# Performance work log

Hardware: AMD Instinct MI355X
Metric: run time of the kernel (lower is better)

The kernel has to match this reference:

```python
import jax, jax.numpy as jnp
import numpy as np

B, S, H, N = 2, 2048, 1024, 16
D = H // N


def setup_inputs() -> dict:
    key = jax.random.key(0)
    k1, k2, k3 = jax.random.split(key, 3)
    # Xavier-uniform-ish init for projection weights
    lim_in = (6.0 / (H + 3 * H)) ** 0.5
    lim_out = (6.0 / (H + H)) ** 0.5
    return {
        "hidden_states": jax.random.normal(k1, (B, S, H), dtype=jnp.float32),
        "w_in": jax.random.uniform(k2, (3 * H, H), minval=-lim_in, maxval=lim_in, dtype=jnp.float32),
        "b_in": jnp.zeros((3 * H,), dtype=jnp.float32),
        "w_out": jax.random.uniform(k3, (H, H), minval=-lim_out, maxval=lim_out, dtype=jnp.float32),
        "b_out": jnp.zeros((H,), dtype=jnp.float32),
    }


def reference(hidden_states, w_in, b_in, w_out, b_out):
    b, s, h = hidden_states.shape
    qkv = hidden_states @ w_in.T + b_in  # [B,S,3H]
    q, k, v = jnp.split(qkv, 3, axis=-1)
    # [B,S,H] -> [B,N,S,D]
    def to_heads(x):
        return x.reshape(b, s, N, D).transpose(0, 2, 1, 3)
    q, k, v = to_heads(q), to_heads(k), to_heads(v)
    scale = D ** -0.5
    scores = jnp.einsum("bnqd,bnkd->bnqk", q, k) * scale  # [B,N,S,S]
    causal = jnp.triu(jnp.ones((s, s), dtype=bool), k=1)
    scores = jnp.where(causal, -jnp.inf, scores)
    attn = jax.nn.softmax(scores, axis=-1)
    out = jnp.einsum("bnqk,bnkd->bnqd", attn, v)  # [B,N,S,D]
    out = out.transpose(0, 2, 1, 3).reshape(b, s, h)
    return out @ w_out.T + b_out
```

## Files before the change

### kernel.cpp

```cpp
#include <hip/hip_runtime.h>
#include <hip/hip_bf16.h>

#define BB 2
#define SS 2048
#define HH 1024
#define NH 16
#define DD 64
#define H3 3072
#define MM (BB*SS)

typedef unsigned short u16;
typedef unsigned int u32;
typedef __attribute__((ext_vector_type(8))) short bf16x8;
typedef __attribute__((ext_vector_type(4))) float f32x4;

__device__ __forceinline__ u16 f2bf(float f) {
    union { float f; u32 u; } v; v.f = f;
    u32 u = v.u;
    u += 0x7fffu + ((u >> 16) & 1u);
    return (u16)(u >> 16);
}
__device__ __forceinline__ float bf2f(u16 h) {
    union { u32 u; float f; } v; v.u = ((u32)h) << 16;
    return v.f;
}
__device__ __forceinline__ u32 pack2bf(float a, float b) {
    __hip_bfloat162 h = __float22bfloat162_rn(float2{a, b});
    u32 u; __builtin_memcpy(&u, &h, 4);
    return u;
}
__device__ __forceinline__ void gl_lds16(const void* g, void* l) {
    __builtin_amdgcn_global_load_lds(
        (const __attribute__((address_space(1))) u32*)g,
        (__attribute__((address_space(3))) u32*)l, 16, 0, 0);
}

__global__ void cvt3bf(const float4* __restrict__ s0, uint2* __restrict__ d0, int n0,
                       const float4* __restrict__ s1, uint2* __restrict__ d1, int n1,
                       const float4* __restrict__ s2, uint2* __restrict__ d2, int n2) {
    int i = blockIdx.x * blockDim.x + threadIdx.x;
    const int tot = n0 + n1 + n2;
    for (; i < tot; i += gridDim.x * blockDim.x) {
        const float4* s; uint2* d; int j;
        if (i < n0)            { s = s0; d = d0; j = i; }
        else if (i < n0 + n1)  { s = s1; d = d1; j = i - n0; }
        else                   { s = s2; d = d2; j = i - n0 - n1; }
        float4 v = s[j];
        uint2 o; o.x = pack2bf(v.x, v.y); o.y = pack2bf(v.z, v.w);
        d[j] = o;
    }
}

template<int BN, int MODE>
__global__ __launch_bounds__(256, 2)
void gemm_k2(const u16* __restrict__ A, const u16* __restrict__ Bbf,
             const u16* __restrict__ biasbf, void* __restrict__ Cptr,
             u16* __restrict__ Qo, u16* __restrict__ Ko, u16* __restrict__ Vto,
             int M, int Nn, int K)
{
    constexpr int NFR = BN / 32;
    __shared__ __align__(16) u16 Alds[128 * 32];
    __shared__ __align__(16) u16 Blds[BN * 32];
    const int tid = threadIdx.x;
    const int w = tid >> 6, lane = tid & 63, quad = lane >> 4, l16 = lane & 15;
    const int m0 = blockIdx.x * 128, n0 = blockIdx.y * BN;
    const int wm = w >> 1, wn = w & 1;
    const int rA4 = lane >> 2, c8b = (lane & 3) * 8;

    f32x4 acc[4][NFR] = {};

    for (int k0 = 0; k0 < K; k0 += 32) {
        __syncthreads();
#pragma unroll
        for (int q = 0; q < 2; ++q) {
            int row0 = w * 32 + q * 16;
            gl_lds16(&A[(size_t)(m0 + row0 + rA4) * K + k0 + c8b], &Alds[row0 * 32]);
        }
#pragma unroll
        for (int q = 0; q < BN / 64; ++q) {
            int row0 = w * (BN / 4) + q * 16;
            gl_lds16(&Bbf[(size_t)(n0 + row0 + rA4) * K + k0 + c8b], &Blds[row0 * 32]);
        }
        __syncthreads();

        bf16x8 af[4], bfr[NFR];
#pragma unroll
        for (int mi = 0; mi < 4; ++mi)
            af[mi] = *(const bf16x8*)&Alds[(wm * 64 + mi * 16 + l16) * 32 + quad * 8];
#pragma unroll
        for (int ni = 0; ni < NFR; ++ni)
            bfr[ni] = *(const bf16x8*)&Blds[(wn * (BN / 2) + ni * 16 + l16) * 32 + quad * 8];
#pragma unroll
        for (int mi = 0; mi < 4; ++mi)
#pragma unroll
            for (int ni = 0; ni < NFR; ++ni)
                acc[mi][ni] = __builtin_amdgcn_mfma_f32_16x16x32_bf16(
                    af[mi], bfr[ni], acc[mi][ni], 0, 0, 0);
    }

#pragma unroll
    for (int mi = 0; mi < 4; ++mi) {
        int row_b = m0 + wm * 64 + mi * 16 + quad * 4;
#pragma unroll
        for (int ni = 0; ni < NFR; ++ni) {
            int col = n0 + wn * (BN / 2) + ni * 16 + l16;
            float bv = bf2f(biasbf[col]);
            if constexpr (MODE == 1) {
#pragma unroll
                for (int i = 0; i < 4; ++i)
                    ((float*)Cptr)[(size_t)(row_b + i) * Nn + col] = acc[mi][ni][i] + bv;
            } else {
                if (col < 1024) {
#pragma unroll
                    for (int i = 0; i < 4; ++i)
                        Qo[(size_t)(row_b + i) * 1024 + col] =
                            f2bf((acc[mi][ni][i] + bv) * 0.125f);
                } else if (col < 2048) {
#pragma unroll
                    for (int i = 0; i < 4; ++i)
                        Ko[(size_t)(row_b + i) * 1024 + (col - 1024)] =
                            f2bf(acc[mi][ni][i] + bv);
                } else {
                    int d = col - 2048, hh = d >> 6, dd = d & 63;
                    int b = row_b >> 11, s = row_b & 2047;
                    u16 t0 = f2bf(acc[mi][ni][0] + bv), t1 = f2bf(acc[mi][ni][1] + bv);
                    u16 t2 = f2bf(acc[mi][ni][2] + bv), t3 = f2bf(acc[mi][ni][3] + bv);
                    uint2 pk; pk.x = (u32)t0 | ((u32)t1 << 16);
                    pk.y = (u32)t2 | ((u32)t3 << 16);
                    *(uint2*)&Vto[((size_t)((b * 16 + hh) * 64 + dd)) * 2048 + s] = pk;
                }
            }
        }
    }
}

__global__ __launch_bounds__(256, 2)
void attn_v4(const u16* __restrict__ Q, const u16* __restrict__ Kb,
             const u16* __restrict__ Vt, u16* __restrict__ attn_out) {
    const int pr = blockIdx.x, h = blockIdx.y, b = blockIdx.z;
    const int tid = threadIdx.x;
    const int w = tid >> 6, lane = tid & 63, quad = lane >> 4, l16 = lane & 15;
    __shared__ __align__(16) u16 Klds[2][64 * 72];
    __shared__ __align__(16) u16 Vlds[2][64 * 72];
    const int r0 = tid >> 3, cc8 = (tid & 7) * 8;
    const int Rp = ((r0 & 4) << 2) | ((r0 & 24) >> 1) | (r0 & 3);

    for (int half = 0; half < 2; ++half) {
        const int qt = half ? pr : (31 - pr);
        const int q0 = qt * 64;
        const int T = qt + 1;

        const u16* Qb = Q  + (size_t)(b * SS + q0) * 1024 + h * 64;
        const u16* Kg = Kb + (size_t)(b * SS) * 1024 + h * 64;
        const u16* Vg = Vt + (size_t)((b * 16 + h) * 64) * 2048;

        bf16x8 qf0 = *(const bf16x8*)&Qb[(size_t)(w * 16 + l16) * 1024 + quad * 8];
        bf16x8 qf1 = *(const bf16x8*)&Qb[(size_t)(w * 16 + l16) * 1024 + 32 + quad * 8];

        f32x4 oacc[4] = {};
        float lp = 0.f;

        uint4 kr0 = *(const uint4*)&Kg[(size_t)r0 * 1024 + cc8];
        uint4 kr1 = *(const uint4*)&Kg[(size_t)(r0 + 32) * 1024 + cc8];
        uint4 vr0 = *(const uint4*)&Vg[(size_t)r0 * 2048 + cc8];
        uint4 vr1 = *(const uint4*)&Vg[(size_t)(r0 + 32) * 2048 + cc8];
        __syncthreads();
        *(uint4*)&Klds[0][Rp * 72 + cc8]        = kr0;
        *(uint4*)&Klds[0][(Rp + 32) * 72 + cc8] = kr1;
        *(uint4*)&Vlds[0][r0 * 72 + cc8]        = vr0;
        *(uint4*)&Vlds[0][(r0 + 32) * 72 + cc8] = vr1;

        for (int t = 0; t < T; ++t) {
            const int cur = t & 1;
            __syncthreads();
            if (t + 1 < T) {
                const int nv = (t + 1) * 64;
                kr0 = *(const uint4*)&Kg[(size_t)(nv + r0) * 1024 + cc8];
                kr1 = *(const uint4*)&Kg[(size_t)(nv + r0 + 32) * 1024 + cc8];
                vr0 = *(const uint4*)&Vg[(size_t)r0 * 2048 + nv + cc8];
                vr1 = *(const uint4*)&Vg[(size_t)(r0 + 32) * 2048 + nv + cc8];
            }
            f32x4 sacc[4] = {};
#pragma unroll
            for (int ni = 0; ni < 4; ++ni) {
                bf16x8 kf0 = *(const bf16x8*)&Klds[cur][(ni * 16 + l16) * 72 + quad * 8];
                bf16x8 kf1 = *(const bf16x8*)&Klds[cur][(ni * 16 + l16) * 72 + 32 + quad * 8];
                sacc[ni] = __builtin_amdgcn_mfma_f32_16x16x32_bf16(kf0, qf0, sacc[ni], 0, 0, 0);
                sacc[ni] = __builtin_amdgcn_mfma_f32_16x16x32_bf16(kf1, qf1, sacc[ni], 0, 0, 0);
            }
            u32 pk[4][2];
            if (t + 1 < T) {
#pragma unroll
                for (int ni = 0; ni < 4; ++ni) {
                    float p0 = __expf(sacc[ni][0]), p1 = __expf(sacc[ni][1]);
                    float p2 = __expf(sacc[ni][2]), p3 = __expf(sacc[ni][3]);
                    lp += (p0 + p1) + (p2 + p3);
                    pk[ni][0] = pack2bf(p0, p1);
                    pk[ni][1] = pack2bf(p2, p3);
                }
            } else {
                const int thr = w * 16 + l16;
#pragma unroll
                for (int ni = 0; ni < 4; ++ni) {
                    const int pb = 32 * (ni >> 1) + 8 * quad + 4 * (ni & 1);
                    float pv[4];
#pragma unroll
                    for (int i = 0; i < 4; ++i) {
                        float e = __expf(sacc[ni][i]);
                        pv[i] = (pb + i <= thr) ? e : 0.f;
                    }
                    lp += (pv[0] + pv[1]) + (pv[2] + pv[3]);
                    pk[ni][0] = pack2bf(pv[0], pv[1]);
                    pk[ni][1] = pack2bf(pv[2], pv[3]);
                }
            }
            union { u32 u[4]; bf16x8 v; } pf0, pf1;
            pf0.u[0] = pk[0][0]; pf0.u[1] = pk[0][1];
            pf0.u[2] = pk[1][0]; pf0.u[3] = pk[1][1];
            pf1.u[0] = pk[2][0]; pf1.u[1] = pk[2][1];
            pf1.u[2] = pk[3][0]; pf1.u[3] = pk[3][1];
#pragma unroll
            for (int ni = 0; ni < 4; ++ni) {
                bf16x8 vf0 = *(const bf16x8*)&Vlds[cur][(ni * 16 + l16) * 72 + quad * 8];
                bf16x8 vf1 = *(const bf16x8*)&Vlds[cur][(ni * 16 + l16) * 72 + 32 + quad * 8];
                oacc[ni] = __builtin_amdgcn_mfma_f32_16x16x32_bf16(pf0.v, vf0, oacc[ni], 0, 0, 0);
                oacc[ni] = __builtin_amdgcn_mfma_f32_16x16x32_bf16(pf1.v, vf1, oacc[ni], 0, 0, 0);
            }
            if (t + 1 < T) {
                const int nxt = cur ^ 1;
                *(uint4*)&Klds[nxt][Rp * 72 + cc8]        = kr0;
                *(uint4*)&Klds[nxt][(Rp + 32) * 72 + cc8] = kr1;
                *(uint4*)&Vlds[nxt][r0 * 72 + cc8]        = vr0;
                *(uint4*)&Vlds[nxt][(r0 + 32) * 72 + cc8] = vr1;
            }
        }

        lp += __shfl_xor(lp, 16, 64);
        lp += __shfl_xor(lp, 32, 64);
        float linv[4];
#pragma unroll
        for (int i = 0; i < 4; ++i)
            linv[i] = 1.0f / __shfl(lp, quad * 4 + i, 64);

        u16* ob = attn_out + (size_t)(b * SS + q0 + w * 16) * 1024 + h * 64;
#pragma unroll
        for (int ni = 0; ni < 4; ++ni)
#pragma unroll
            for (int i = 0; i < 4; ++i)
                ob[(size_t)(quad * 4 + i) * 1024 + ni * 16 + l16] =
                    f2bf(oacc[ni][i] * linv[i]);
    }
}

extern "C" void kernel_launch(void* const* d_in, const int* in_sizes, int n_in,
                              void* d_out, int out_size, void* d_ws, size_t ws_size,
                              hipStream_t stream) {
    const float* hidden = (const float*)d_in[0];
    const float* w_in   = (const float*)d_in[1];
    const float* b_in   = (const float*)d_in[2];
    const float* w_out  = (const float*)d_in[3];
    const float* b_out  = (const float*)d_in[4];
    float* out = (float*)d_out;

    char* ws = (char*)d_ws;
    u16* hid_bf  = (u16*)d_out;
    u16* wi_bf   = (u16*)ws;
    u16* bi_bf   = (u16*)(ws + 6291456);
    u16* attn_ws = (u16*)ws;
    u16* Qbuf    = (u16*)(ws + 8388608);
    u16* wo_bf   = (u16*)(ws + 8388608);
    u16* bo_bf   = (u16*)(ws + 8388608 + 2097152);
    u16* Kbuf    = (u16*)(ws + 16777216);
    u16* Vtbuf   = (u16*)(ws + 25165824);

    cvt3bf<<<dim3(2048), dim3(256), 0, stream>>>(
        (const float4*)hidden, (uint2*)hid_bf, 1048576,
        (const float4*)w_in,   (uint2*)wi_bf,  786432,
        (const float4*)b_in,   (uint2*)bi_bf,  768);
    gemm_k2<128, 2><<<dim3(32, 24), dim3(256), 0, stream>>>(
        hid_bf, wi_bf, bi_bf, nullptr, Qbuf, Kbuf, Vtbuf, MM, H3, HH);
    attn_v4<<<dim3(16, NH, BB), dim3(256), 0, stream>>>(
        Qbuf, Kbuf, Vtbuf, attn_ws);
    cvt3bf<<<dim3(512), dim3(256), 0, stream>>>(
        (const float4*)w_out, (uint2*)wo_bf, 262144,
        (const float4*)b_out, (uint2*)bo_bf, 256,
        nullptr, nullptr, 0);
    gemm_k2<64, 1><<<dim3(32, 16), dim3(256), 0, stream>>>(
        attn_ws, wo_bf, bo_bf, out, nullptr, nullptr, nullptr, MM, HH, HH);
}
```

Measured before the change: 178.9 us.

## Stage attention K/V tiles with direct global-to-LDS loads and XOR swizzle

The attention kernel now moves K and V tiles straight from global memory into LDS with global_load_lds instead of staging them through registers. Padded 72-element LDS rows become unpadded 64-element rows with an XOR swizzle to avoid bank conflicts. The grid is flattened to 1D with a remapping that interleaves heads and batches across block IDs. This aims to cut register pressure and VGPR-to-LDS store instructions, at the cost of relying on the global_load_lds prefetch being complete at the next barrier and on intricate swizzle index math.

```diff
diff --git a/kernel.cpp b/kernel.cpp
--- a/kernel.cpp
+++ b/kernel.cpp
@@ -33,6 +33,9 @@
     __builtin_amdgcn_global_load_lds(
         (const __attribute__((address_space(1))) u32*)g,
         (__attribute__((address_space(3))) u32*)l, 16, 0, 0);
+}
+__device__ __forceinline__ int ginv(int R) {
+    return (R & 35) | ((R & 8) << 1) | ((R & 4) << 1) | ((R & 16) >> 2);
 }
 
 __global__ void cvt3bf(const float4* __restrict__ s0, uint2* __restrict__ d0, int n0,
@@ -135,15 +138,24 @@
 }
 
 __global__ __launch_bounds__(256, 2)
-void attn_v4(const u16* __restrict__ Q, const u16* __restrict__ Kb,
+void attn_v5(const u16* __restrict__ Q, const u16* __restrict__ Kb,
              const u16* __restrict__ Vt, u16* __restrict__ attn_out) {
-    const int pr = blockIdx.x, h = blockIdx.y, b = blockIdx.z;
+    const int bid = blockIdx.x;
+    const int r8 = bid & 7, qq = bid >> 3;
+    const int pr = qq >> 2, g = (qq & 3) * 8 + r8;
+    const int h = g & 15, b = g >> 4;
     const int tid = threadIdx.x;
     const int w = tid >> 6, lane = tid & 63, quad = lane >> 4, l16 = lane & 15;
-    __shared__ __align__(16) u16 Klds[2][64 * 72];
-    __shared__ __align__(16) u16 Vlds[2][64 * 72];
-    const int r0 = tid >> 3, cc8 = (tid & 7) * 8;
-    const int Rp = ((r0 & 4) << 2) | ((r0 & 24) >> 1) | (r0 & 3);
+    __shared__ __align__(16) u16 Klds[2][64 * 64];
+    __shared__ __align__(16) u16 Vlds[2][64 * 64];
+
+    const int sl = lane >> 3, cch = lane & 7;
+    const int rho0 = (2 * w) * 8 + sl, rho1 = (2 * w + 1) * 8 + sl;
+    const int gcs = (cch ^ sl) * 8;
+    const int kg0 = ginv(rho0), kg1 = ginv(rho1);
+    const int ls0 = (2 * w) * 512, ls1 = (2 * w + 1) * 512;
+    const int xk0 = (quad ^ (l16 & 7)) * 8;
+    const int xk1 = ((quad + 4) ^ (l16 & 7)) * 8;
 
     for (int half = 0; half < 2; ++half) {
         const int qt = half ? pr : (31 - pr);
@@ -154,37 +166,34 @@
         const u16* Kg = Kb + (size_t)(b * SS) * 1024 + h * 64;
         const u16* Vg = Vt + (size_t)((b * 16 + h) * 64) * 2048;
 
+#define STAGE_T(kv0_, bi_) do {                                               \
+        gl_lds16(&Kg[(size_t)((kv0_) + kg0) * 1024 + gcs], &Klds[bi_][ls0]);  \
+        gl_lds16(&Kg[(size_t)((kv0_) + kg1) * 1024 + gcs], &Klds[bi_][ls1]);  \
+        gl_lds16(&Vg[(size_t)rho0 * 2048 + (kv0_) + gcs], &Vlds[bi_][ls0]);   \
+        gl_lds16(&Vg[(size_t)rho1 * 2048 + (kv0_) + gcs], &Vlds[bi_][ls1]);   \
+    } while (0)
+
         bf16x8 qf0 = *(const bf16x8*)&Qb[(size_t)(w * 16 + l16) * 1024 + quad * 8];
         bf16x8 qf1 = *(const bf16x8*)&Qb[(size_t)(w * 16 + l16) * 1024 + 32 + quad * 8];
 
         f32x4 oacc[4] = {};
         float lp = 0.f;
 
-        uint4 kr0 = *(const uint4*)&Kg[(size_t)r0 * 1024 + cc8];
-        uint4 kr1 = *(const uint4*)&Kg[(size_t)(r0 + 32) * 1024 + cc8];
-        uint4 vr0 = *(const uint4*)&Vg[(size_t)r0 * 2048 + cc8];
-        uint4 vr1 = *(const uint4*)&Vg[(size_t)(r0 + 32) * 2048 + cc8];
         __syncthreads();
-        *(uint4*)&Klds[0][Rp * 72 + cc8]        = kr0;
-        *(uint4*)&Klds[0][(Rp + 32) * 72 + cc8] = kr1;
-        *(uint4*)&Vlds[0][r0 * 72 + cc8]        = vr0;
-        *(uint4*)&Vlds[0][(r0 + 32) * 72 + cc8] = vr1;
+        STAGE_T(0, 0);
 
         for (int t = 0; t < T; ++t) {
             const int cur = t & 1;
             __syncthreads();
-            if (t + 1 < T) {
-                const int nv = (t + 1) * 64;
-                kr0 = *(const uint4*)&Kg[(size_t)(nv + r0) * 1024 + cc8];
-                kr1 = *(const uint4*)&Kg[(size_t)(nv + r0 + 32) * 1024 + cc8];
-                vr0 = *(const uint4*)&Vg[(size_t)r0 * 2048 + nv + cc8];
-                vr1 = *(const uint4*)&Vg[(size_t)(r0 + 32) * 2048 + nv + cc8];
-            }
+            if (t + 1 < T) STAGE_T((t + 1) * 64, cur ^ 1);
+            const u16* Kc = Klds[cur];
+            const u16* Vc = Vlds[cur];
             f32x4 sacc[4] = {};
 #pragma unroll
             for (int ni = 0; ni < 4; ++ni) {
-                bf16x8 kf0 = *(const bf16x8*)&Klds[cur][(ni * 16 + l16) * 72 + quad * 8];
-                bf16x8 kf1 = *(const bf16x8*)&Klds[cur][(ni * 16 + l16) * 72 + 32 + quad * 8];
+                const int rb = (ni * 16 + l16) * 64;
+                bf16x8 kf0 = *(const bf16x8*)&Kc[rb + xk0];
+                bf16x8 kf1 = *(const bf16x8*)&Kc[rb + xk1];
                 sacc[ni] = __builtin_amdgcn_mfma_f32_16x16x32_bf16(kf0, qf0, sacc[ni], 0, 0, 0);
                 sacc[ni] = __builtin_amdgcn_mfma_f32_16x16x32_bf16(kf1, qf1, sacc[ni], 0, 0, 0);
             }
@@ -221,17 +230,11 @@
             pf1.u[2] = pk[3][0]; pf1.u[3] = pk[3][1];
 #pragma unroll
             for (int ni = 0; ni < 4; ++ni) {
-                bf16x8 vf0 = *(const bf16x8*)&Vlds[cur][(ni * 16 + l16) * 72 + quad * 8];
-                bf16x8 vf1 = *(const bf16x8*)&Vlds[cur][(ni * 16 + l16) * 72 + 32 + quad * 8];
+                const int rb = (ni * 16 + l16) * 64;
+                bf16x8 vf0 = *(const bf16x8*)&Vc[rb + xk0];
+                bf16x8 vf1 = *(const bf16x8*)&Vc[rb + xk1];
                 oacc[ni] = __builtin_amdgcn_mfma_f32_16x16x32_bf16(pf0.v, vf0, oacc[ni], 0, 0, 0);
                 oacc[ni] = __builtin_amdgcn_mfma_f32_16x16x32_bf16(pf1.v, vf1, oacc[ni], 0, 0, 0);
-            }
-            if (t + 1 < T) {
-                const int nxt = cur ^ 1;
-                *(uint4*)&Klds[nxt][Rp * 72 + cc8]        = kr0;
-                *(uint4*)&Klds[nxt][(Rp + 32) * 72 + cc8] = kr1;
-                *(uint4*)&Vlds[nxt][r0 * 72 + cc8]        = vr0;
-                *(uint4*)&Vlds[nxt][(r0 + 32) * 72 + cc8] = vr1;
             }
         }
 
@@ -249,6 +252,7 @@
             for (int i = 0; i < 4; ++i)
                 ob[(size_t)(quad * 4 + i) * 1024 + ni * 16 + l16] =
                     f2bf(oacc[ni][i] * linv[i]);
+#undef STAGE_T
     }
 }
 
@@ -279,7 +283,7 @@
         (const float4*)b_in,   (uint2*)bi_bf,  768);
     gemm_k2<128, 2><<<dim3(32, 24), dim3(256), 0, stream>>>(
         hid_bf, wi_bf, bi_bf, nullptr, Qbuf, Kbuf, Vtbuf, MM, H3, HH);
-    attn_v4<<<dim3(16, NH, BB), dim3(256), 0, stream>>>(
+    attn_v5<<<dim3(512), dim3(256), 0, stream>>>(
         Qbuf, Kbuf, Vtbuf, attn_ws);
     cvt3bf<<<dim3(512), dim3(256), 0, stream>>>(
         (const float4*)w_out, (uint2*)wo_bf, 262144,
```

Result: no change. 177.2 us (-0.9%).
